# Performance work log

Hardware: AMD Instinct MI355X
Metric: run time of the kernel (lower is better)

## Reference

```python
import jax, jax.numpy as jnp
import numpy as np

# Mamba hyperparams (mamba_ssm defaults for d_model=128)
D_MODEL = 128
DEPTH = 8
D_INNER = 256   # expand=2
D_STATE = 16
D_CONV = 4
DT_RANK = 8     # ceil(D_MODEL/16)
EPS = 1e-5


def setup_inputs() -> dict:
    key = jax.random.key(0)
    ks = jax.random.split(key, 8)
    B, H, W = 1, 48, 48
    s = lambda k, shape, sc=0.02: jax.random.normal(k, shape, jnp.float32) * sc
    return {
        "x": jax.random.normal(ks[0], (B, D_MODEL, H, W), jnp.float32),
        "W_in": s(ks[1], (DEPTH, D_MODEL, 2 * D_INNER)),
        "conv_w": s(ks[2], (DEPTH, D_INNER, D_CONV), 0.2),
        "conv_b": jnp.zeros((DEPTH, D_INNER), jnp.float32),
        "W_xproj": s(ks[3], (DEPTH, D_INNER, DT_RANK + 2 * D_STATE)),
        "W_dt": s(ks[4], (DEPTH, DT_RANK, D_INNER), 0.1),
        "b_dt": jnp.full((DEPTH, D_INNER), -4.6, jnp.float32),  # softplus ~= 0.01
        "A_log": jnp.broadcast_to(
            jnp.log(jnp.arange(1, D_STATE + 1, dtype=jnp.float32)),
            (DEPTH, D_INNER, D_STATE)).copy(),
        "D_skip": jnp.ones((DEPTH, D_INNER), jnp.float32),
        "W_out": s(ks[5], (DEPTH, D_INNER, D_MODEL)),
        "rms_w": jnp.ones((DEPTH, D_MODEL), jnp.float32),
    }


def _rmsnorm(x, w):
    return x * jax.lax.rsqrt(jnp.mean(x * x, axis=-1, keepdims=True) + EPS) * w


def _mamba_layer(x, Wi, cw, cb, Wx, Wdt, bdt, Alog, Dp, Wo):
    # x: [B, L, D_MODEL]
    B, L, _ = x.shape
    xz = x @ Wi                                   # [B, L, 2*d_inner]
    xi, z = jnp.split(xz, 2, axis=-1)
    # causal depthwise conv1d, kernel D_CONV
    xp = jnp.pad(xi, ((0, 0), (D_CONV - 1, 0), (0, 0)))
    xc = sum(xp[:, k:k + L, :] * cw[:, k] for k in range(D_CONV)) + cb
    xc = jax.nn.silu(xc)                          # [B, L, d_inner]
    dbl = xc @ Wx                                 # [B, L, dt_rank + 2*d_state]
    dt_r = dbl[..., :DT_RANK]
    Bs = dbl[..., DT_RANK:DT_RANK + D_STATE]      # [B, L, d_state]
    Cs = dbl[..., DT_RANK + D_STATE:]
    dt = jax.nn.softplus(dt_r @ Wdt + bdt)        # [B, L, d_inner]
    A = -jnp.exp(Alog)                            # [d_inner, d_state]
    dA = jnp.exp(dt[..., None] * A)               # [B, L, d_inner, d_state]
    dBx = (dt * xc)[..., None] * Bs[:, :, None, :]
    # linear recurrence h_t = dA_t * h_{t-1} + dBx_t via parallel scan
    def comb(l, r):
        al, bl = l
        ar, br = r
        return ar * al, ar * bl + br
    _, h = jax.lax.associative_scan(comb, (dA, dBx), axis=1)
    y = jnp.einsum('blds,bls->bld', h, Cs) + Dp * xc
    y = y * jax.nn.silu(z)
    return y @ Wo                                 # [B, L, D_MODEL]


def reference(x, W_in, conv_w, conv_b, W_xproj, W_dt, b_dt, A_log, D_skip, W_out, rms_w):
    B, C, H, W = x.shape
    seq = x.reshape(B, C, H * W).transpose(0, 2, 1)  # [B, L, C]
    for l in range(DEPTH):
        seq = _mamba_layer(seq, W_in[l], conv_w[l], conv_b[l], W_xproj[l],
                           W_dt[l], b_dt[l], A_log[l], D_skip[l], W_out[l])
        seq = _rmsnorm(seq, rms_w[l])
    return seq.reshape(B, H, W, C).transpose(0, 3, 1, 2)
```

## Files before the change

### kernel.cpp

```cpp
#include <hip/hip_runtime.h>
#include <math.h>

#define LSEQ 2304
#define DM 128
#define DI 256
#define DS 16
#define RK 8
#define NCH 576
#define CLEN 4
#define NG 24
#define GS 24
#define NSI (DI*DS)
#define EPSF 1e-5f

__device__ __forceinline__ float silu_f(float s) { return s / (1.f + __expf(-s)); }
__device__ __forceinline__ float softplus_f(float x) { return (x > 20.f) ? x : log1pf(__expf(x)); }

template<bool FIRST>
__global__ __launch_bounds__(256, 4)
void k_in(const float* __restrict__ seq, const float* __restrict__ x0,
          const float* __restrict__ Wi,
          const float* __restrict__ cw, const float* __restrict__ cbias,
          float* __restrict__ xc_g, float* __restrict__ sz_g) {
    __shared__ float As[11 * 128];
    const int l0 = blockIdx.x * 8;
    const int half = blockIdx.y & 1;
    const bool isZ = blockIdx.y >= 2;
    const int tid = threadIdx.x;

    for (int idx = tid; idx < 11 * 128; idx += 256) {
        const int r = idx >> 7, cc = idx & 127;
        const int l = l0 - 3 + r;
        As[idx] = (l >= 0) ? (FIRST ? x0[cc * LSEQ + l] : seq[l * DM + cc]) : 0.f;
    }
    __syncthreads();

    const int c = tid & 127;
    const int rg = tid >> 7;
    const int d = half * 128 + c;

    if (!isZ) {
        float ax[7] = {0.f, 0.f, 0.f, 0.f, 0.f, 0.f, 0.f};
        for (int k4 = 0; k4 < 32; ++k4) {
            float bv[4];
#pragma unroll
            for (int u = 0; u < 4; ++u) bv[u] = Wi[(k4 * 4 + u) * 512 + d];
#pragma unroll
            for (int r = 0; r < 7; ++r) {
                const float4 a4 = *(const float4*)&As[(rg * 4 + r) * 128 + k4 * 4];
                ax[r] += a4.x * bv[0] + a4.y * bv[1] + a4.z * bv[2] + a4.w * bv[3];
            }
        }
        const float w0 = cw[d * 4 + 0], w1 = cw[d * 4 + 1];
        const float w2 = cw[d * 4 + 2], w3 = cw[d * 4 + 3];
        const float cbv = cbias[d];
#pragma unroll
        for (int rr = 0; rr < 4; ++rr) {
            const float v = silu_f(cbv + w0 * ax[rr] + w1 * ax[rr + 1] +
                                   w2 * ax[rr + 2] + w3 * ax[rr + 3]);
            xc_g[(l0 + rg * 4 + rr) * DI + d] = v;
        }
    } else {
        float az[4] = {0.f, 0.f, 0.f, 0.f};
        for (int k4 = 0; k4 < 32; ++k4) {
            float bv[4];
#pragma unroll
            for (int u = 0; u < 4; ++u) bv[u] = Wi[(k4 * 4 + u) * 512 + 256 + d];
#pragma unroll
            for (int r = 0; r < 4; ++r) {
                const float4 a4 = *(const float4*)&As[(rg * 4 + r + 3) * 128 + k4 * 4];
                az[r] += a4.x * bv[0] + a4.y * bv[1] + a4.z * bv[2] + a4.w * bv[3];
            }
        }
#pragma unroll
        for (int rr = 0; rr < 4; ++rr)
            sz_g[(l0 + rg * 4 + rr) * DI + d] = silu_f(az[rr]);
    }
}

__global__ __launch_bounds__(256, 2)
void k_mid2(const float* __restrict__ xc_g,
            const float* __restrict__ Wx,
            const float* __restrict__ Wdt, const float* __restrict__ bdt,
            const float* __restrict__ Alog,
            float* __restrict__ dbl_g, float* __restrict__ dt_g,
            float* __restrict__ P, float* __restrict__ S) {
    __shared__ float xcs[CLEN * 256];
    __shared__ float dtrs[CLEN * 8];
    __shared__ float dbls[CLEN * 32];
    const int c = blockIdx.x;
    const int l0 = c * CLEN;
    const int tid = threadIdx.x;
    const int d = tid;

    ((float4*)xcs)[tid] = ((const float4*)&xc_g[l0 * DI])[tid];
    __syncthreads();

    if (tid < CLEN * 40) {
        const int r = tid / 40, j = tid - r * 40;
        const float* xr = &xcs[r * 256];
        float acc = 0.f;
#pragma unroll 8
        for (int k = 0; k < DI; ++k) acc += xr[k] * Wx[k * 40 + j];
        if (j < RK) dtrs[r * 8 + j] = acc;
        else {
            dbls[r * 32 + (j - 8)] = acc;
            dbl_g[(l0 + r) * 32 + (j - 8)] = acc;
        }
    }
    __syncthreads();

    float dtv[CLEN], xcv[CLEN];
    {
        float wdt[8];
#pragma unroll
        for (int q = 0; q < 8; ++q) wdt[q] = Wdt[q * DI + d];
        const float bdv = bdt[d];
#pragma unroll
        for (int r = 0; r < CLEN; ++r) {
            float acc = bdv;
#pragma unroll
            for (int q = 0; q < 8; ++q) acc += dtrs[r * 8 + q] * wdt[q];
            dtv[r] = softplus_f(acc);
            dt_g[(l0 + r) * DI + d] = dtv[r];
            xcv[r] = xcs[r * 256 + d];
        }
    }

    float A[16], pr[16], hs[16];
#pragma unroll
    for (int v = 0; v < 4; ++v) {
        const float4 a4 = *(const float4*)&Alog[d * DS + v * 4];
        A[v * 4 + 0] = -__expf(a4.x);
        A[v * 4 + 1] = -__expf(a4.y);
        A[v * 4 + 2] = -__expf(a4.z);
        A[v * 4 + 3] = -__expf(a4.w);
    }
#pragma unroll
    for (int s = 0; s < 16; ++s) { pr[s] = 1.f; hs[s] = 0.f; }
#pragma unroll
    for (int t = 0; t < CLEN; ++t) {
        const float dtt = dtv[t];
        const float uv = dtt * xcv[t];
        const float* Brow = &dbls[t * 32];
#pragma unroll
        for (int s = 0; s < 16; ++s) {
            const float e = __expf(dtt * A[s]);
            pr[s] *= e;
            hs[s] = e * hs[s] + uv * Brow[s];
        }
    }
    const int base = c * NSI + d * DS;
#pragma unroll
    for (int v = 0; v < 4; ++v) {
        *(float4*)&P[base + v * 4] =
            make_float4(pr[v * 4], pr[v * 4 + 1], pr[v * 4 + 2], pr[v * 4 + 3]);
        *(float4*)&S[base + v * 4] =
            make_float4(hs[v * 4], hs[v * 4 + 1], hs[v * 4 + 2], hs[v * 4 + 3]);
    }
}

__global__ __launch_bounds__(256, 4)
void k_carry1(float* __restrict__ P, float* __restrict__ S,
              float* __restrict__ Pg, float* __restrict__ Sg) {
    const int g = blockIdx.x;
    const int i = blockIdx.y * 256 + threadIdx.x;
    float G = 0.f, Pp = 1.f;
    const int base = g * GS * NSI + i;
#pragma unroll 8
    for (int k = 0; k < GS; ++k) {
        const int idx = base + k * NSI;
        const float p = P[idx];
        const float s = S[idx];
        S[idx] = G;
        P[idx] = Pp;
        G = p * G + s;
        Pp *= p;
    }
    Pg[g * NSI + i] = Pp;
    Sg[g * NSI + i] = G;
}

__global__ __launch_bounds__(256, 4)
void k_carry2(const float* __restrict__ Pg, float* __restrict__ Sg) {
    const int i = blockIdx.x * 256 + threadIdx.x;
    float G = 0.f;
#pragma unroll 8
    for (int g = 0; g < NG; ++g) {
        const int idx = g * NSI + i;
        const float p = Pg[idx];
        const float s = Sg[idx];
        Sg[idx] = G;
        G = p * G + s;
    }
}

template<bool LAST>
__global__ __launch_bounds__(256, 2)
void k_tail(const float* __restrict__ dt_g, const float* __restrict__ xc_g,
            const float* __restrict__ dbl_g, const float* __restrict__ Alog,
            const float* __restrict__ Sloc, const float* __restrict__ Ppre,
            const float* __restrict__ Gc, const float* __restrict__ Dp,
            const float* __restrict__ sz_g, const float* __restrict__ Wo,
            const float* __restrict__ rmsw, float* __restrict__ seq,
            float* __restrict__ out) {
    __shared__ float dbls[CLEN * 32];
    __shared__ float Ys[CLEN * 256];
    __shared__ float Os[CLEN * 129];
    __shared__ float red[CLEN * 32];
    __shared__ float scaleS[CLEN];
    const int c = blockIdx.x;
    const int g = c / GS;
    const int l0 = c * CLEN;
    const int tid = threadIdx.x;
    const int d = tid;

    if (tid < CLEN * 32) dbls[tid] = dbl_g[l0 * 32 + tid];

    float A[16], h[16];
#pragma unroll
    for (int v = 0; v < 4; ++v) {
        const float4 a4 = *(const float4*)&Alog[d * DS + v * 4];
        A[v * 4 + 0] = -__expf(a4.x);
        A[v * 4 + 1] = -__expf(a4.y);
        A[v * 4 + 2] = -__expf(a4.z);
        A[v * 4 + 3] = -__expf(a4.w);
        const float4 s4 = *(const float4*)&Sloc[c * NSI + d * DS + v * 4];
        const float4 p4 = *(const float4*)&Ppre[c * NSI + d * DS + v * 4];
        const float4 g4 = *(const float4*)&Gc[g * NSI + d * DS + v * 4];
        h[v * 4 + 0] = s4.x + p4.x * g4.x;
        h[v * 4 + 1] = s4.y + p4.y * g4.y;
        h[v * 4 + 2] = s4.z + p4.z * g4.z;
        h[v * 4 + 3] = s4.w + p4.w * g4.w;
    }
    float dtv[CLEN], xcv[CLEN], szv[CLEN];
#pragma unroll
    for (int r = 0; r < CLEN; ++r) {
        dtv[r] = dt_g[(l0 + r) * DI + d];
        xcv[r] = xc_g[(l0 + r) * DI + d];
        szv[r] = sz_g[(l0 + r) * DI + d];
    }
    const float dskip = Dp[d];
    __syncthreads();
#pragma unroll
    for (int t = 0; t < CLEN; ++t) {
        const float dtt = dtv[t];
        const float uv = dtt * xcv[t];
        float sum = 0.f;
#pragma unroll
        for (int s = 0; s < 16; ++s) {
            const float e = __expf(dtt * A[s]);
            h[s] = e * h[s] + uv * dbls[t * 32 + s];
            sum += h[s] * dbls[t * 32 + 16 + s];
        }
        Ys[t * 256 + d] = (sum + dskip * xcv[t]) * szv[t];
    }
    __syncthreads();

    {
        const int cc = tid & 127;
        const int kg = tid >> 7;
        const int k0 = kg * 128;
        float acc[CLEN] = {0.f, 0.f, 0.f, 0.f};
#pragma unroll 4
        for (int k = k0; k < k0 + 128; ++k) {
            const float w = Wo[k * DM + cc];
#pragma unroll
            for (int r = 0; r < CLEN; ++r) acc[r] += Ys[r * 256 + k] * w;
        }
        if (kg == 0) {
#pragma unroll
            for (int r = 0; r < CLEN; ++r) Os[r * 129 + cc] = acc[r];
        }
        __syncthreads();
        if (kg == 1) {
#pragma unroll
            for (int r = 0; r < CLEN; ++r) Os[r * 129 + cc] += acc[r];
        }
        __syncthreads();
    }

    if (tid < CLEN * 32) {
        const int r = tid >> 5, part = tid & 31;
        float ss = 0.f;
#pragma unroll
        for (int i = 0; i < 4; ++i) {
            const float v = Os[r * 129 + part * 4 + i];
            ss += v * v;
        }
        red[tid] = ss;
    }
    __syncthreads();
    if (tid < CLEN) {
        float ss = 0.f;
#pragma unroll
        for (int p = 0; p < 32; ++p) ss += red[tid * 32 + p];
        scaleS[tid] = rsqrtf(ss * (1.f / DM) + EPSF);
    }
    __syncthreads();
    if (LAST) {
        for (int idx = tid; idx < CLEN * DM; idx += 256) {
            const int r = idx >> 7, cc = idx & 127;
            out[cc * LSEQ + (l0 + r)] = Os[r * 129 + cc] * scaleS[r] * rmsw[cc];
        }
    } else {
        for (int idx = tid; idx < CLEN * DM; idx += 256) {
            const int r = idx >> 7, cc = idx & 127;
            seq[(l0 + r) * DM + cc] = Os[r * 129 + cc] * scaleS[r] * rmsw[cc];
        }
    }
}

extern "C" void kernel_launch(void* const* d_in, const int* in_sizes, int n_in,
                              void* d_out, int out_size, void* d_ws, size_t ws_size,
                              hipStream_t stream) {
    const float* x    = (const float*)d_in[0];
    const float* W_in = (const float*)d_in[1];
    const float* cw   = (const float*)d_in[2];
    const float* cb   = (const float*)d_in[3];
    const float* Wx   = (const float*)d_in[4];
    const float* Wdt  = (const float*)d_in[5];
    const float* bdt  = (const float*)d_in[6];
    const float* Alog = (const float*)d_in[7];
    const float* Dp   = (const float*)d_in[8];
    const float* Wo   = (const float*)d_in[9];
    const float* rmsw = (const float*)d_in[10];
    float* out = (float*)d_out;

    float* ws   = (float*)d_ws;
    float* seq  = ws; ws += LSEQ * DM;
    float* szb  = ws; ws += LSEQ * DI;
    float* xcb  = ws; ws += LSEQ * DI;
    float* dtb  = ws; ws += LSEQ * DI;
    float* dblb = ws; ws += LSEQ * 32;
    float* Pb   = ws; ws += NCH * NSI;
    float* Sb   = ws; ws += NCH * NSI;
    float* Pgb  = ws; ws += NG * NSI;
    float* Sgb  = ws; ws += NG * NSI;

    for (int layer = 0; layer < 8; ++layer) {
        const float* Wi_l   = W_in + (size_t)layer * DM * 512;
        const float* cw_l   = cw   + (size_t)layer * DI * 4;
        const float* cb_l   = cb   + (size_t)layer * DI;
        const float* Wx_l   = Wx   + (size_t)layer * DI * 40;
        const float* Wdt_l  = Wdt  + (size_t)layer * RK * DI;
        const float* bdt_l  = bdt  + (size_t)layer * DI;
        const float* Alog_l = Alog + (size_t)layer * DI * DS;
        const float* Dp_l   = Dp   + (size_t)layer * DI;
        const float* Wo_l   = Wo   + (size_t)layer * DI * DM;
        const float* rmsw_l = rmsw + (size_t)layer * DM;

        if (layer == 0)
            k_in<true><<<dim3(288, 4), 256, 0, stream>>>(seq, x, Wi_l, cw_l, cb_l,
                                                         xcb, szb);
        else
            k_in<false><<<dim3(288, 4), 256, 0, stream>>>(seq, x, Wi_l, cw_l, cb_l,
                                                          xcb, szb);

        k_mid2<<<NCH, 256, 0, stream>>>(xcb, Wx_l, Wdt_l, bdt_l, Alog_l,
                                        dblb, dtb, Pb, Sb);

        k_carry1<<<dim3(NG, 16), 256, 0, stream>>>(Pb, Sb, Pgb, Sgb);
        k_carry2<<<16, 256, 0, stream>>>(Pgb, Sgb);

        if (layer == 7)
            k_tail<true><<<NCH, 256, 0, stream>>>(dtb, xcb, dblb, Alog_l, Sb, Pb,
                                                  Sgb, Dp_l, szb, Wo_l, rmsw_l,
                                                  seq, out);
        else
            k_tail<false><<<NCH, 256, 0, stream>>>(dtb, xcb, dblb, Alog_l, Sb, Pb,
                                                   Sgb, Dp_l, szb, Wo_l, rmsw_l,
                                                   seq, out);
    }
}
```

Before: 631.6 us.

## Split small GEMV reductions across all threads and fuse carry kernels via atomics

Measured after the change: 1.036 ms. 64.0% more time.

```diff
diff --git a/kernel.cpp b/kernel.cpp
--- a/kernel.cpp
+++ b/kernel.cpp
@@ -78,7 +78,7 @@
     }
 }
 
-__global__ __launch_bounds__(256, 2)
+__global__ __launch_bounds__(256, 4)
 void k_mid2(const float* __restrict__ xc_g,
             const float* __restrict__ Wx,
             const float* __restrict__ Wdt, const float* __restrict__ bdt,
@@ -86,6 +86,7 @@
             float* __restrict__ dbl_g, float* __restrict__ dt_g,
             float* __restrict__ P, float* __restrict__ S) {
     __shared__ float xcs[CLEN * 256];
+    __shared__ float part[4 * 160];
     __shared__ float dtrs[CLEN * 8];
     __shared__ float dbls[CLEN * 32];
     const int c = blockIdx.x;
@@ -96,12 +97,21 @@
     ((float4*)xcs)[tid] = ((const float4*)&xc_g[l0 * DI])[tid];
     __syncthreads();
 
-    if (tid < CLEN * 40) {
-        const int r = tid / 40, j = tid - r * 40;
-        const float* xr = &xcs[r * 256];
+    for (int task = tid; task < 640; task += 256) {
+        const int kc = task / 160;
+        const int o = task - kc * 160;
+        const int r = o / 40, j = o - r * 40;
+        const float* xr = &xcs[r * 256 + kc * 64];
+        const float* wp = &Wx[(kc * 64) * 40 + j];
         float acc = 0.f;
 #pragma unroll 8
-        for (int k = 0; k < DI; ++k) acc += xr[k] * Wx[k * 40 + j];
+        for (int k = 0; k < 64; ++k) acc += xr[k] * wp[k * 40];
+        part[kc * 160 + o] = acc;
+    }
+    __syncthreads();
+    if (tid < 160) {
+        const float acc = part[tid] + part[160 + tid] + part[320 + tid] + part[480 + tid];
+        const int r = tid / 40, j = tid - r * 40;
         if (j < RK) dtrs[r * 8 + j] = acc;
         else {
             dbls[r * 32 + (j - 8)] = acc;
@@ -160,34 +170,42 @@
     }
 }
 
-__global__ __launch_bounds__(256, 4)
-void k_carry1(float* __restrict__ P, float* __restrict__ S,
-              float* __restrict__ Pg, float* __restrict__ Sg) {
+__global__ __launch_bounds__(256, 2)
+void k_carry(float* __restrict__ P, float* __restrict__ S,
+             float* __restrict__ Pg, float* __restrict__ Sg,
+             unsigned int* __restrict__ ctr, unsigned int target) {
     const int g = blockIdx.x;
-    const int i = blockIdx.y * 256 + threadIdx.x;
-    float G = 0.f, Pp = 1.f;
-    const int base = g * GS * NSI + i;
+    const int y = blockIdx.y;
+    const int i = y * 256 + threadIdx.x;
+    {
+        float G = 0.f, Pp = 1.f;
+        const int base = g * GS * NSI + i;
 #pragma unroll 8
-    for (int k = 0; k < GS; ++k) {
-        const int idx = base + k * NSI;
-        const float p = P[idx];
-        const float s = S[idx];
-        S[idx] = G;
-        P[idx] = Pp;
-        G = p * G + s;
-        Pp *= p;
-    }
-    Pg[g * NSI + i] = Pp;
-    Sg[g * NSI + i] = G;
-}
-
-__global__ __launch_bounds__(256, 4)
-void k_carry2(const float* __restrict__ Pg, float* __restrict__ Sg) {
-    const int i = blockIdx.x * 256 + threadIdx.x;
+        for (int k = 0; k < GS; ++k) {
+            const int idx = base + k * NSI;
+            const float p = P[idx];
+            const float s = S[idx];
+            S[idx] = G;
+            P[idx] = Pp;
+            G = p * G + s;
+            Pp *= p;
+        }
+        Pg[g * NSI + i] = Pp;
+        Sg[g * NSI + i] = G;
+    }
+    __threadfence();
+    __syncthreads();
+    if (threadIdx.x == 0) atomicAdd(&ctr[y], 1u);
+    if (g != 0) return;
+    if (threadIdx.x == 0) {
+        while (atomicAdd(&ctr[y], 0u) < target) __builtin_amdgcn_s_sleep(8);
+    }
+    __syncthreads();
+    __threadfence();
     float G = 0.f;
 #pragma unroll 8
-    for (int g = 0; g < NG; ++g) {
-        const int idx = g * NSI + i;
+    for (int gg = 0; gg < NG; ++gg) {
+        const int idx = gg * NSI + i;
         const float p = Pg[idx];
         const float s = Sg[idx];
         Sg[idx] = G;
@@ -206,6 +224,7 @@
             float* __restrict__ out) {
     __shared__ float dbls[CLEN * 32];
     __shared__ float Ys[CLEN * 256];
+    __shared__ float partO[4 * CLEN * 128];
     __shared__ float Os[CLEN * 129];
     __shared__ float red[CLEN * 32];
     __shared__ float scaleS[CLEN];
@@ -258,24 +277,35 @@
     __syncthreads();
 
     {
-        const int cc = tid & 127;
-        const int kg = tid >> 7;
-        const int k0 = kg * 128;
-        float acc[CLEN] = {0.f, 0.f, 0.f, 0.f};
-#pragma unroll 4
-        for (int k = k0; k < k0 + 128; ++k) {
-            const float w = Wo[k * DM + cc];
-#pragma unroll
-            for (int r = 0; r < CLEN; ++r) acc[r] += Ys[r * 256 + k] * w;
-        }
-        if (kg == 0) {
-#pragma unroll
-            for (int r = 0; r < CLEN; ++r) Os[r * 129 + cc] = acc[r];
+        const int ccp = tid & 63;
+        const int kg = tid >> 6;
+        float acc[CLEN][2];
+#pragma unroll
+        for (int r = 0; r < CLEN; ++r) { acc[r][0] = 0.f; acc[r][1] = 0.f; }
+        const float* wp = &Wo[(kg * 64) * DM + ccp * 2];
+        const float* yp = &Ys[kg * 64];
+#pragma unroll 8
+        for (int k = 0; k < 64; ++k) {
+            const float2 w2 = *(const float2*)(wp + k * DM);
+#pragma unroll
+            for (int r = 0; r < CLEN; ++r) {
+                const float yv = yp[r * 256 + k];
+                acc[r][0] += yv * w2.x;
+                acc[r][1] += yv * w2.y;
+            }
+        }
+#pragma unroll
+        for (int r = 0; r < CLEN; ++r) {
+            partO[(kg * CLEN + r) * 128 + ccp * 2 + 0] = acc[r][0];
+            partO[(kg * CLEN + r) * 128 + ccp * 2 + 1] = acc[r][1];
         }
         __syncthreads();
-        if (kg == 1) {
-#pragma unroll
-            for (int r = 0; r < CLEN; ++r) Os[r * 129 + cc] += acc[r];
+        for (int idx = tid; idx < CLEN * 128; idx += 256) {
+            const int r = idx >> 7, cc = idx & 127;
+            Os[r * 129 + cc] = partO[(0 * CLEN + r) * 128 + cc] +
+                               partO[(1 * CLEN + r) * 128 + cc] +
+                               partO[(2 * CLEN + r) * 128 + cc] +
+                               partO[(3 * CLEN + r) * 128 + cc];
         }
         __syncthreads();
     }
@@ -337,6 +367,9 @@
     float* Sb   = ws; ws += NCH * NSI;
     float* Pgb  = ws; ws += NG * NSI;
     float* Sgb  = ws; ws += NG * NSI;
+    unsigned int* ctr = (unsigned int*)ws;
+
+    hipMemsetAsync(ctr, 0, 16 * sizeof(unsigned int), stream);
 
     for (int layer = 0; layer < 8; ++layer) {
         const float* Wi_l   = W_in + (size_t)layer * DM * 512;
@@ -360,8 +393,8 @@
         k_mid2<<<NCH, 256, 0, stream>>>(xcb, Wx_l, Wdt_l, bdt_l, Alog_l,
                                         dblb, dtb, Pb, Sb);
 
-        k_carry1<<<dim3(NG, 16), 256, 0, stream>>>(Pb, Sb, Pgb, Sgb);
-        k_carry2<<<16, 256, 0, stream>>>(Pgb, Sgb);
+        k_carry<<<dim3(NG, 16), 256, 0, stream>>>(Pb, Sb, Pgb, Sgb, ctr,
+                                                  24u * (unsigned)(layer + 1));
 
         if (layer == 7)
             k_tail<true><<<NCH, 256, 0, stream>>>(dtb, xcb, dblb, Alog_l, Sb, Pb,
```
